# Performance work log

Measured on AMD Instinct MI355X. Metric: run time of the kernel, lower is better.

The kernel has to match this reference:

```python
import jax, jax.numpy as jnp
import numpy as np

N_EMBED = 384
NUM_EXPERTS = 8
TOP_K = 2


def setup_inputs() -> dict:
    key = jax.random.key(0)
    k_x, k_n, k_w1, k_b1, k_w2, k_b2 = jax.random.split(key, 6)
    B, T = 16, 4096
    bound = 1.0 / np.sqrt(N_EMBED)
    return {
        "x": jax.random.normal(k_x, (B, T, N_EMBED), dtype=jnp.float32),
        "noise": jax.random.normal(k_n, (B, T, NUM_EXPERTS), dtype=jnp.float32),
        "w_route": jax.random.uniform(k_w1, (NUM_EXPERTS, N_EMBED), jnp.float32, -bound, bound),
        "b_route": jax.random.uniform(k_b1, (NUM_EXPERTS,), jnp.float32, -bound, bound),
        "w_noise": jax.random.uniform(k_w2, (NUM_EXPERTS, N_EMBED), jnp.float32, -bound, bound),
        "b_noise": jax.random.uniform(k_b2, (NUM_EXPERTS,), jnp.float32, -bound, bound),
    }


def reference(x, noise, w_route, b_route, w_noise, b_noise):
    # two tiny linears: [B,T,D] @ [D,E] -> [B,T,E]
    logits = jnp.einsum("btd,ed->bte", x, w_route) + b_route
    noise_logits = jnp.einsum("btd,ed->bte", x, w_noise) + b_noise
    noisy_logits = logits + noise * jax.nn.softplus(noise_logits)

    top_k_logits, indices = jax.lax.top_k(noisy_logits, TOP_K)  # [B,T,k]

    # scatter top-k values into a -inf tensor; equivalently mask non-topk to -inf
    # (values at the top-k positions are exactly the noisy logits there)
    mask = jax.nn.one_hot(indices, NUM_EXPERTS, dtype=jnp.bool_).any(axis=-2)  # [B,T,E]
    sparse_logits = jnp.where(mask, noisy_logits, -jnp.inf)
    router_output = jax.nn.softmax(sparse_logits, axis=-1)
    return router_output, indices
```

## Files before the change

kernel.cpp:

```cpp
#include <hip/hip_runtime.h>
#include <math.h>


constexpr int D  = 384;
constexpr int NW = 16 * D;

__global__ __launch_bounds__(256) void noisy_topk_router_f32(
    const float* __restrict__ x,
    const float* __restrict__ noise,
    const float* __restrict__ w_route,
    const float* __restrict__ b_route,
    const float* __restrict__ w_noise,
    const float* __restrict__ b_noise,
    float* __restrict__ out,
    int ntok)
{
    __shared__ float w_lds[NW];
    __shared__ float bias[16];

    const int tid = threadIdx.x;

#pragma unroll
    for (int r = 0; r < 3; ++r) {
        int i = (tid + 256 * r) * 4;
        *(float4*)(w_lds + i)        = *(const float4*)(w_route + i);
        *(float4*)(w_lds + 3072 + i) = *(const float4*)(w_noise + i);
    }
    if (tid < 8)            bias[tid] = b_route[tid];
    else if (tid < 16)      bias[tid] = b_noise[tid - 8];
    __syncthreads();

    const int wave = tid >> 6;
    const int lane = tid & 63;
    const int tg   = lane >> 2;
    const int c    = lane & 3;
    const int token = blockIdx.x * 64 + wave * 16 + tg;

    float acc[16];
#pragma unroll
    for (int e = 0; e < 16; ++e) acc[e] = 0.f;

    const float* xrow = x + (size_t)token * D;
#pragma unroll 6
    for (int j = 0; j < 24; ++j) {
        const int dbase = j * 16 + c * 4;
        float4 xv = *(const float4*)(xrow + dbase);
#pragma unroll
        for (int e = 0; e < 16; ++e) {
            float4 wv = *(const float4*)(w_lds + e * D + dbase);
            acc[e] += xv.x * wv.x + xv.y * wv.y + xv.z * wv.z + xv.w * wv.w;
        }
    }

#pragma unroll
    for (int e = 0; e < 16; ++e) {
        acc[e] += __shfl_xor(acc[e], 1);
        acc[e] += __shfl_xor(acc[e], 2);
    }

    if (c == 0) {
        float4 n0 = *(const float4*)(noise + (size_t)token * 8);
        float4 n1 = *(const float4*)(noise + (size_t)token * 8 + 4);
        float nz[8] = {n0.x, n0.y, n0.z, n0.w, n1.x, n1.y, n1.z, n1.w};

        float noisy[8];
#pragma unroll
        for (int e = 0; e < 8; ++e) {
            float lg = acc[e] + bias[e];
            float nl = acc[8 + e] + bias[8 + e];
            float sp = fmaxf(nl, 0.f) + log1pf(expf(-fabsf(nl)));
            noisy[e] = lg + nz[e] * sp;
        }

        float v0 = noisy[0]; int i0 = 0;
#pragma unroll
        for (int e = 1; e < 8; ++e)
            if (noisy[e] > v0) { v0 = noisy[e]; i0 = e; }
        float v1 = -INFINITY; int i1 = 0;
#pragma unroll
        for (int e = 0; e < 8; ++e)
            if (e != i0 && noisy[e] > v1) { v1 = noisy[e]; i1 = e; }

        float ex  = expf(v1 - v0);
        float inv = 1.f / (1.f + ex);
        float p0  = inv;
        float p1  = ex * inv;

        float pr[8];
#pragma unroll
        for (int e = 0; e < 8; ++e)
            pr[e] = (e == i0) ? p0 : ((e == i1) ? p1 : 0.f);

        float* orow = out + (size_t)token * 8;
        *(float4*)(orow)     = make_float4(pr[0], pr[1], pr[2], pr[3]);
        *(float4*)(orow + 4) = make_float4(pr[4], pr[5], pr[6], pr[7]);

        float2 iv = make_float2((float)i0, (float)i1);
        *(float2*)(out + (size_t)ntok * 8 + (size_t)token * 2) = iv;
    }
}

extern "C" void kernel_launch(void* const* d_in, const int* in_sizes, int n_in,
                              void* d_out, int out_size, void* d_ws, size_t ws_size,
                              hipStream_t stream) {
    const float* x       = (const float*)d_in[0];
    const float* noise   = (const float*)d_in[1];
    const float* w_route = (const float*)d_in[2];
    const float* b_route = (const float*)d_in[3];
    const float* w_noise = (const float*)d_in[4];
    const float* b_noise = (const float*)d_in[5];
    float* out = (float*)d_out;

    const int ntok   = in_sizes[0] / D;
    const int blocks = ntok / 64;

    hipLaunchKernelGGL(noisy_topk_router_f32, dim3(blocks), dim3(256), 0, stream,
                       x, noise, w_route, b_route, w_noise, b_noise, out, ntok);
}
```

Before: 172.1 us.

## Register-block four tokens per thread to reuse LDS weight reads

Each thread now accumulates dot products for four tokens instead of one. Eight lanes split the embedding dimension, and a three-step shuffle reduction combines their partial sums. Every float4 of weights read from LDS is applied to four x rows, cutting LDS traffic per FLOP, which looks like the bottleneck of the previous layout. In exchange the kernel uses more registers, launches half as many blocks, and indexes the accumulators with a runtime lane index in the epilogue, which may add selects or scratch spills.

```diff
diff --git a/kernel.cpp b/kernel.cpp
--- a/kernel.cpp
+++ b/kernel.cpp
@@ -2,8 +2,7 @@
 #include <math.h>
 
 
-constexpr int D  = 384;
-constexpr int NW = 16 * D;
+constexpr int D = 384;
 
 __global__ __launch_bounds__(256) void noisy_topk_router_f32(
     const float* __restrict__ x,
@@ -15,7 +14,7 @@
     float* __restrict__ out,
     int ntok)
 {
-    __shared__ float w_lds[NW];
+    __shared__ float w_lds[16 * D];
     __shared__ float bias[16];
 
     const int tid = threadIdx.x;
@@ -23,42 +22,54 @@
 #pragma unroll
     for (int r = 0; r < 3; ++r) {
         int i = (tid + 256 * r) * 4;
-        *(float4*)(w_lds + i)        = *(const float4*)(w_route + i);
-        *(float4*)(w_lds + 3072 + i) = *(const float4*)(w_noise + i);
+        *(float4*)(w_lds + i)            = *(const float4*)(w_route + i);
+        *(float4*)(w_lds + 3072 + i)     = *(const float4*)(w_noise + i);
     }
-    if (tid < 8)            bias[tid] = b_route[tid];
-    else if (tid < 16)      bias[tid] = b_noise[tid - 8];
+    if (tid < 8)       bias[tid] = b_route[tid];
+    else if (tid < 16) bias[tid] = b_noise[tid - 8];
     __syncthreads();
 
     const int wave = tid >> 6;
     const int lane = tid & 63;
-    const int tg   = lane >> 2;
-    const int c    = lane & 3;
-    const int token = blockIdx.x * 64 + wave * 16 + tg;
+    const int tg   = lane >> 3;
+    const int c    = lane & 7;
+    const int tok0 = blockIdx.x * 128 + wave * 32 + tg * 4;
 
-    float acc[16];
+    float acc[4][16];
 #pragma unroll
-    for (int e = 0; e < 16; ++e) acc[e] = 0.f;
+    for (int t = 0; t < 4; ++t)
+#pragma unroll
+        for (int e = 0; e < 16; ++e) acc[t][e] = 0.f;
 
-    const float* xrow = x + (size_t)token * D;
-#pragma unroll 6
-    for (int j = 0; j < 24; ++j) {
-        const int dbase = j * 16 + c * 4;
-        float4 xv = *(const float4*)(xrow + dbase);
+    const float* xbase = x + (size_t)tok0 * D + c * 4;
+#pragma unroll 2
+    for (int j = 0; j < 12; ++j) {
+        const int dbase = j * 32;
+        float4 xv0 = *(const float4*)(xbase + dbase);
+        float4 xv1 = *(const float4*)(xbase + D + dbase);
+        float4 xv2 = *(const float4*)(xbase + 2 * D + dbase);
+        float4 xv3 = *(const float4*)(xbase + 3 * D + dbase);
 #pragma unroll
         for (int e = 0; e < 16; ++e) {
-            float4 wv = *(const float4*)(w_lds + e * D + dbase);
-            acc[e] += xv.x * wv.x + xv.y * wv.y + xv.z * wv.z + xv.w * wv.w;
+            float4 wv = *(const float4*)(w_lds + e * D + dbase + c * 4);
+            acc[0][e] += xv0.x * wv.x + xv0.y * wv.y + xv0.z * wv.z + xv0.w * wv.w;
+            acc[1][e] += xv1.x * wv.x + xv1.y * wv.y + xv1.z * wv.z + xv1.w * wv.w;
+            acc[2][e] += xv2.x * wv.x + xv2.y * wv.y + xv2.z * wv.z + xv2.w * wv.w;
+            acc[3][e] += xv3.x * wv.x + xv3.y * wv.y + xv3.z * wv.z + xv3.w * wv.w;
         }
     }
 
 #pragma unroll
-    for (int e = 0; e < 16; ++e) {
-        acc[e] += __shfl_xor(acc[e], 1);
-        acc[e] += __shfl_xor(acc[e], 2);
-    }
+    for (int t = 0; t < 4; ++t)
+#pragma unroll
+        for (int e = 0; e < 16; ++e) {
+            acc[t][e] += __shfl_xor(acc[t][e], 1);
+            acc[t][e] += __shfl_xor(acc[t][e], 2);
+            acc[t][e] += __shfl_xor(acc[t][e], 4);
+        }
 
-    if (c == 0) {
+    if (c < 4) {
+        const int token = tok0 + c;
         float4 n0 = *(const float4*)(noise + (size_t)token * 8);
         float4 n1 = *(const float4*)(noise + (size_t)token * 8 + 4);
         float nz[8] = {n0.x, n0.y, n0.z, n0.w, n1.x, n1.y, n1.z, n1.w};
@@ -66,8 +77,8 @@
         float noisy[8];
 #pragma unroll
         for (int e = 0; e < 8; ++e) {
-            float lg = acc[e] + bias[e];
-            float nl = acc[8 + e] + bias[8 + e];
+            float lg = acc[c][e] + bias[e];
+            float nl = acc[c][8 + e] + bias[8 + e];
             float sp = fmaxf(nl, 0.f) + log1pf(expf(-fabsf(nl)));
             noisy[e] = lg + nz[e] * sp;
         }
@@ -95,8 +106,8 @@
         *(float4*)(orow)     = make_float4(pr[0], pr[1], pr[2], pr[3]);
         *(float4*)(orow + 4) = make_float4(pr[4], pr[5], pr[6], pr[7]);
 
-        float2 iv = make_float2((float)i0, (float)i1);
-        *(float2*)(out + (size_t)ntok * 8 + (size_t)token * 2) = iv;
+        *(float2*)(out + (size_t)ntok * 8 + (size_t)token * 2) =
+            make_float2((float)i0, (float)i1);
     }
 }
 
@@ -112,7 +123,7 @@
     float* out = (float*)d_out;
 
     const int ntok   = in_sizes[0] / D;
-    const int blocks = ntok / 64;
+    const int blocks = ntok / 128;
 
     hipLaunchKernelGGL(noisy_topk_router_f32, dim3(blocks), dim3(256), 0, stream,
                        x, noise, w_route, b_route, w_noise, b_noise, out, ntok);
```

Measured after the change: 181.7 us. 1.06x slower.
